# Performance work log

Measured on AMD Instinct MI355X. Metric: run time of the kernel, lower is better.

The kernel has to match this reference:

```python
import jax, jax.numpy as jnp
import numpy as np

GRID = (8192, 8192)   # 2D lattice, *dims
NDIM = 2              # links.shape[0]
P_LINK = 0.45         # subcritical bond probability -> finite clusters, bounded step count


def setup_inputs() -> dict:
    key = jax.random.key(0)
    k1, k2 = jax.random.split(key)
    # links[i] marks an open bond between site x and its +1 neighbour along axis i
    links = jax.random.uniform(k1, (NDIM,) + GRID) < P_LINK
    seed_idx = jax.random.randint(k2, (NDIM,), 0, GRID[0]).astype(jnp.int32)
    return {"links": links, "seed_idx": seed_idx}


def _flood_fill(links, seed_idx):
    """Faithful port of ClusterSelection.from_seed_idx: BFS-style roll+mask
    expansion iterated to fixed point via lax.while_loop."""
    ndim = links.shape[0]
    grid = links.shape[1:]
    selected0 = jnp.zeros(grid, dtype=bool).at[tuple(seed_idx)].set(True)

    def cond(carry):
        _, is_done, _ = carry
        return ~is_done

    def body(carry):
        sel0, _, steps = carry
        sel = sel0
        for i in range(ndim):  # unrolled over the (small, static) ndim
            # sites whose -1-neighbour or self is selected can use bond i
            links_to_try = sel0 | jnp.roll(sel0, -1, i)
            links_sel = links_to_try & links[i]
            # a taken bond marks both of its endpoints
            links_sel = links_sel | jnp.roll(links_sel, 1, i)
            sel = sel | links_sel
        is_done = (sel ^ sel0).sum() == 0
        return sel, is_done, steps + 1

    sel, _, steps = jax.lax.while_loop(
        cond, body, (selected0, jnp.array(False), jnp.array(0, jnp.int32))
    )
    return sel, steps


def reference(links, seed_idx):
    sel, _steps = _flood_fill(links, seed_idx)
    return sel
```

## Files before the change

kernel.cpp:

```cpp
#include <hip/hip_runtime.h>
#include <stdint.h>

#define GW 8192
#define GMASK 8191
#define PLANE 67108864ULL
#define TPD 128
#define TMASK 127
#define NTILES 16384
#define QCAP 16384
#define QMASK 16383
#define WPR 128

typedef unsigned long long u64;
typedef unsigned int u32;

__global__ void clear_bitmap_kernel(uint4* __restrict__ p, int n) {
    int i = blockIdx.x * blockDim.x + threadIdx.x;
    if (i < n) p[i] = make_uint4(0, 0, 0, 0);
}

__device__ __forceinline__ u32 nib4(u32 w) {
    return (((w & 0x01010101u) * 0x01020408u) >> 24) & 0xFu;
}
__device__ __forceinline__ u64 pack_row_b8(const unsigned char* p) {
    const uint4* q = (const uint4*)p;
    u64 w = 0;
#pragma unroll
    for (int i = 0; i < 4; i++) {
        uint4 v = q[i];
        u64 nb = (u64)(nib4(v.x) | (nib4(v.y) << 4) | (nib4(v.z) << 8) | (nib4(v.w) << 12));
        w |= nb << (16 * i);
    }
    return w;
}
__device__ __forceinline__ u64 pack_row_b32(const u32* p) {
    u64 w = 0;
#pragma unroll
    for (int k = 0; k < 16; k++) {
        uint4 v = ((const uint4*)p)[k];
        u64 nb = (u64)((v.x != 0) | ((v.y != 0) << 1) | ((v.z != 0) << 2) | ((v.w != 0) << 3));
        w |= nb << (4 * k);
    }
    return w;
}

__global__ void __launch_bounds__(1024)
bfs_tiles_kernel(const unsigned char* __restrict__ links8,
                 const int* __restrict__ seed_idx,
                 u64* __restrict__ bitmap) {
    volatile __shared__ unsigned short q[QCAP];
    __shared__ u32 tflags[NTILES / 32];
    __shared__ int s_qhead, s_qtail, s_active, s_mode, s_c1, s_c3;

    const int tid = threadIdx.x;
    const int ln  = tid & 63;

    for (int i = tid; i < QCAP; i += 1024) q[i] = 0xFFFF;
    for (int i = tid; i < NTILES / 32; i += 1024) tflags[i] = 0;
    if (tid == 0) { s_c1 = 0; s_c3 = 0; s_qhead = 0; s_qtail = 0; s_active = 0; }
    __syncthreads();

    int l1c = 0, l3c = 0;
    for (int i = tid; i < 16384; i += 1024) {
        if (links8[i]) { int m = i & 3; if (m == 1) l1c++; else if (m == 3) l3c++; }
    }
    atomicAdd(&s_c1, l1c);
    atomicAdd(&s_c3, l3c);
    __syncthreads();
    if (tid == 0) {
        s_mode = (s_c1 > 0) ? 0 : ((s_c3 > 0) ? 2 : 1);
        int sr = seed_idx[0] & GMASK, sc = seed_idx[1] & GMASK;
        atomicOr(&bitmap[(u64)sr * WPR + (sc >> 6)], 1ull << (sc & 63));
        int t = (sr >> 6) * TPD + (sc >> 6);
        tflags[t >> 5] = 1u << (t & 31);
        q[0] = (unsigned short)t;
        s_qtail = 1; s_active = 1;
    }
    __syncthreads();

    const int mode = s_mode;
    const unsigned char* p0b = links8;
    const unsigned char* p1b = links8 + PLANE;
    const u32* p0w = (const u32*)links8;
    const u32* p1w = (const u32*)(links8 + PLANE * 4);

    auto enq = [&](int t2) {
        u32 bit = 1u << (t2 & 31);
        u32 old = atomicOr(&tflags[t2 >> 5], bit);
        if (!(old & bit)) {
            atomicAdd(&s_active, 1);
            int pos = atomicAdd(&s_qtail, 1) & QMASK;
            q[pos] = (unsigned short)t2;
        }
    };

    long long guard = 0;
    while (true) {
        int t = -1;
        if (ln == 0) {
            while (true) {
                if (atomicAdd(&s_active, 0) == 0) break;
                int h  = atomicAdd(&s_qhead, 0);
                int tl = atomicAdd(&s_qtail, 0);
                if (h != tl && atomicCAS(&s_qhead, h, h + 1) == h) {
                    int pos = h & QMASK;
                    unsigned short v;
                    long long g2 = 0;
                    while ((v = q[pos]) == 0xFFFF) { if (++g2 > 400000000LL) break; }
                    q[pos] = 0xFFFF;
                    t = v;
                    break;
                }
                if (++guard > 400000000LL) break;
            }
        }
        t = __shfl(t, 0);
        if (t < 0) break;

        const int tR = t >> 7, tC = t & TMASK;
        if (ln == 0) atomicAnd(&tflags[t >> 5], ~(1u << (t & 31)));
        __threadfence_block();

        const int gr = tR * 64 + ln;
        u64* wp = &bitmap[(u64)gr * WPR + tC];
        u64 loaded = *(volatile u64*)wp;

        u64 l0, l1;
        if (mode == 0) {
            l0 = pack_row_b8(p0b + (u64)gr * GW + tC * 64);
            l1 = pack_row_b8(p1b + (u64)gr * GW + tC * 64);
        } else {
            l0 = pack_row_b32(p0w + (u64)gr * GW + tC * 64);
            l1 = pack_row_b32(p1w + (u64)gr * GW + tC * 64);
        }

        u64 P0 = l1 & 0x7FFFFFFFFFFFFFFFull;
        u64 P1 = P0 & (P0 >> 1);
        u64 P2 = P1 & (P1 >> 2);
        u64 P3 = P2 & (P2 >> 4);
        u64 P4 = P3 & (P3 >> 8);
        u64 P5 = P4 & (P4 >> 16);
        u64 D0 = (ln < 63) ? l0 : 0ull;
        u64 D1 = D0 & __shfl_down(D0, 1);
        u64 D2 = D1 & __shfl_down(D1, 2);
        u64 D3 = D2 & __shfl_down(D2, 4);
        u64 D4 = D3 & __shfl_down(D3, 8);
        u64 D5 = D4 & __shfl_down(D4, 16);

        u64 sel = loaded;
        while (true) {
            u64 old = sel;
            sel |= (sel & P0) << 1;  sel |= (sel >> 1)  & P0;
            sel |= (sel & P1) << 2;  sel |= (sel >> 2)  & P1;
            sel |= (sel & P2) << 4;  sel |= (sel >> 4)  & P2;
            sel |= (sel & P3) << 8;  sel |= (sel >> 8)  & P3;
            sel |= (sel & P4) << 16; sel |= (sel >> 16) & P4;
            sel |= (sel & P5) << 32; sel |= (sel >> 32) & P5;
            sel |= __shfl_up(sel & D0, 1);  sel |= __shfl_down(sel, 1)  & D0;
            sel |= __shfl_up(sel & D1, 2);  sel |= __shfl_down(sel, 2)  & D1;
            sel |= __shfl_up(sel & D2, 4);  sel |= __shfl_down(sel, 4)  & D2;
            sel |= __shfl_up(sel & D3, 8);  sel |= __shfl_down(sel, 8)  & D3;
            sel |= __shfl_up(sel & D4, 16); sel |= __shfl_down(sel, 16) & D4;
            sel |= __shfl_up(sel & D5, 32); sel |= __shfl_down(sel, 32) & D5;
            if (__ballot(sel != old) == 0ull) break;
        }

        u64 newbits = sel & ~loaded;
        if (newbits) atomicOr(wp, newbits);

        const int c0 = tC * 64;
        bool rnew = false, lnew = false;
        if ((sel >> 63) & (l1 >> 63) & 1ull) {
            u64 old = atomicOr(&bitmap[(u64)gr * WPR + ((tC + 1) & TMASK)], 1ull);
            rnew = !(old & 1ull);
        }
        {
            u64 lcol = (u64)((c0 - 1) & GMASK);
            bool lopen = (mode == 0) ? (p1b[(u64)gr * GW + lcol] != 0)
                                     : (p1w[(u64)gr * GW + lcol] != 0);
            if ((sel & 1ull) && lopen) {
                u64 old = atomicOr(&bitmap[(u64)gr * WPR + ((tC - 1) & TMASK)], 1ull << 63);
                lnew = !(old & (1ull << 63));
            }
        }
        u64 rmask = __ballot(rnew), lmask = __ballot(lnew);

        const int ga = (tR * 64 - 1) & GMASK;
        bool bopen = (mode == 0) ? (p0b[(u64)ga * GW + c0 + ln] != 0)
                                 : (p0w[(u64)ga * GW + c0 + ln] != 0);
        u64 top_sel = __shfl(sel, 0);
        u64 umask = __ballot(bopen && ((top_sel >> ln) & 1));
        u64 unew = 0;
        if (ln == 0 && umask) {
            u64 old = atomicOr(&bitmap[(u64)ga * WPR + tC], umask);
            unew = umask & ~old;
        }
        u64 dmask = sel & l0;
        const int gb = (tR * 64 + 64) & GMASK;
        u64 dnew = 0;
        if (ln == 63 && dmask) {
            u64 old = atomicOr(&bitmap[(u64)gb * WPR + tC], dmask);
            dnew = dmask & ~old;
        }

        if (ln == 0  && rmask) enq(tR * TPD + ((tC + 1) & TMASK));
        if (ln == 1  && lmask) enq(tR * TPD + ((tC - 1) & TMASK));
        if (ln == 0  && unew)  enq(((tR - 1) & TMASK) * TPD + tC);
        if (ln == 63 && dnew)  enq(((tR + 1) & TMASK) * TPD + tC);

        if (ln == 0) atomicSub(&s_active, 1);
    }
}

__global__ void writeout_kernel(const u64* __restrict__ bitmap, int4* __restrict__ out) {
    int g = blockIdx.x * blockDim.x + threadIdx.x;
    int site0 = g << 2;
    u64 w = bitmap[site0 >> 6];
    u32 b = (u32)(w >> (site0 & 63)) & 0xFu;
    out[g] = make_int4(b & 1, (b >> 1) & 1, (b >> 2) & 1, (b >> 3) & 1);
}

extern "C" void kernel_launch(void* const* d_in, const int* in_sizes, int n_in,
                              void* d_out, int out_size, void* d_ws, size_t ws_size,
                              hipStream_t stream) {
    const unsigned char* links = (const unsigned char*)d_in[0];
    const int* seed = (const int*)d_in[1];

    u64* bitmap = (u64*)((char*)d_ws + 4096);

    clear_bitmap_kernel<<<2048, 256, 0, stream>>>((uint4*)bitmap, 524288);
    bfs_tiles_kernel<<<1, 1024, 0, stream>>>(links, seed, bitmap);
    writeout_kernel<<<65536, 256, 0, stream>>>(bitmap, (int4*)d_out);
}
```

Before: 662.4 us.

## Fuse output zeroing with BFS and keep cluster tiles in shared memory

Replaces the separate bitmap clear and dense output writeout with one mega kernel. Block 0 runs the tile BFS on a shared-memory hash-indexed tile cache, while the other blocks zero the output and the global bitmap concurrently. The final writeout then touches only the visited tiles. If the cluster exceeds the slot capacity, a fallback path uses the global bitmap and a second BFS kernel. This adds spin-wait synchronisation between blocks and relies on the zeroing blocks finishing while block 0 is still resident.

```diff
diff --git a/kernel.cpp b/kernel.cpp
--- a/kernel.cpp
+++ b/kernel.cpp
@@ -7,17 +7,31 @@
 #define TPD 128
 #define TMASK 127
 #define NTILES 16384
+#define WPR 128
+
+#define NSLOT 224
+#define HCAP 1024
+#define HMASK 1023
+#define QC1 2048
+#define QM1 2047
+
 #define QCAP 16384
 #define QMASK 16383
-#define WPR 128
+
+#define WS_FILLDONE 0
+#define WS_OVER 8
+#define WS_GQN 16
+#define WS_NTILES 24
+#define WS_BITMAP 4096
+#define WS_LIST (WS_BITMAP + 8388608)
+#define WS_STAG (WS_LIST + 4096)
+#define WS_GQ (WS_STAG + NSLOT * 512)
+
+#define OUT_U4 16777216u
+#define BM_U4 524288u
 
 typedef unsigned long long u64;
 typedef unsigned int u32;
-
-__global__ void clear_bitmap_kernel(uint4* __restrict__ p, int n) {
-    int i = blockIdx.x * blockDim.x + threadIdx.x;
-    if (i < n) p[i] = make_uint4(0, 0, 0, 0);
-}
 
 __device__ __forceinline__ u32 nib4(u32 w) {
     return (((w & 0x01010101u) * 0x01020408u) >> 24) & 0xFu;
@@ -44,20 +58,51 @@
     return w;
 }
 
+__global__ void clear_ctrl_kernel(unsigned char* ws) {
+    if (threadIdx.x < 16) ((u32*)ws)[threadIdx.x] = 0;
+}
+
 __global__ void __launch_bounds__(1024)
-bfs_tiles_kernel(const unsigned char* __restrict__ links8,
-                 const int* __restrict__ seed_idx,
-                 u64* __restrict__ bitmap) {
-    volatile __shared__ unsigned short q[QCAP];
+mega_kernel(const unsigned char* __restrict__ links8,
+            const int* __restrict__ seed_idx,
+            unsigned char* __restrict__ ws,
+            uint4* __restrict__ outv) {
+    volatile __shared__ unsigned short q[QC1];
     __shared__ u32 tflags[NTILES / 32];
+    __shared__ u32 htab[HCAP];
+    __shared__ u64 selS[NSLOT][64];
+    __shared__ unsigned short slot_tile[NSLOT];
     __shared__ int s_qhead, s_qtail, s_active, s_mode, s_c1, s_c3;
+    __shared__ int s_nslots, s_over, s_gbready;
+
+    if (blockIdx.x != 0) {
+        u32 gtid = (blockIdx.x - 1) * 1024 + threadIdx.x;
+        u32 stride = (gridDim.x - 1) * 1024;
+        uint4 z = make_uint4(0, 0, 0, 0);
+        for (u32 i = gtid; i < OUT_U4; i += stride) outv[i] = z;
+        uint4* bm = (uint4*)(ws + WS_BITMAP);
+        for (u32 i = gtid; i < BM_U4; i += stride) bm[i] = z;
+        __syncthreads();
+        if (threadIdx.x == 0) {
+            __threadfence();
+            atomicAdd((u32*)(ws + WS_FILLDONE), 1u);
+        }
+        return;
+    }
 
     const int tid = threadIdx.x;
-    const int ln  = tid & 63;
-
-    for (int i = tid; i < QCAP; i += 1024) q[i] = 0xFFFF;
+    const int ln = tid & 63;
+    const int wv = tid >> 6;
+
+    for (int i = tid; i < QC1; i += 1024) q[i] = 0xFFFF;
     for (int i = tid; i < NTILES / 32; i += 1024) tflags[i] = 0;
-    if (tid == 0) { s_c1 = 0; s_c3 = 0; s_qhead = 0; s_qtail = 0; s_active = 0; }
+    for (int i = tid; i < HCAP; i += 1024) htab[i] = 0xFFFFFFFFu;
+    for (int i = tid; i < NSLOT; i += 1024) slot_tile[i] = 0xFFFF;
+    for (int i = tid; i < NSLOT * 64; i += 1024) ((u64*)selS)[i] = 0ull;
+    if (tid == 0) {
+        s_c1 = 0; s_c3 = 0; s_qhead = 0; s_qtail = 0; s_active = 0;
+        s_nslots = 0; s_over = 0; s_gbready = 0;
+    }
     __syncthreads();
 
     int l1c = 0, l3c = 0;
@@ -70,8 +115,12 @@
     if (tid == 0) {
         s_mode = (s_c1 > 0) ? 0 : ((s_c3 > 0) ? 2 : 1);
         int sr = seed_idx[0] & GMASK, sc = seed_idx[1] & GMASK;
-        atomicOr(&bitmap[(u64)sr * WPR + (sc >> 6)], 1ull << (sc & 63));
         int t = (sr >> 6) * TPD + (sc >> 6);
+        s_nslots = 1;
+        slot_tile[0] = (unsigned short)t;
+        u32 h = ((u32)t * 2654435761u) >> 22;
+        htab[h & HMASK] = (u32)t;
+        selS[0][sr & 63] = 1ull << (sc & 63);
         tflags[t >> 5] = 1u << (t & 31);
         q[0] = (unsigned short)t;
         s_qtail = 1; s_active = 1;
@@ -83,14 +132,58 @@
     const unsigned char* p1b = links8 + PLANE;
     const u32* p0w = (const u32*)links8;
     const u32* p1w = (const u32*)(links8 + PLANE * 4);
-
+    u64* bitmap = (u64*)(ws + WS_BITMAP);
+    const u32 nfill = gridDim.x - 1;
+
+    auto find_slot = [&](int t) -> int {
+        u32 h = ((u32)t * 2654435761u) >> 22;
+        for (int i = 0; i < HCAP; i++) {
+            u32 e = ((volatile u32*)htab)[(h + i) & HMASK];
+            if (e == 0xFFFFFFFFu) return -1;
+            if ((e & 0x3FFFu) == (u32)t) return (int)(e >> 14);
+        }
+        return -1;
+    };
+    auto find_or_alloc = [&](int t) -> int {
+        u32 h = ((u32)t * 2654435761u) >> 22;
+        for (int i = 0; i < HCAP; i++) {
+            int idx = (int)((h + i) & HMASK);
+            u32 e = ((volatile u32*)htab)[idx];
+            if (e == 0xFFFFFFFFu) {
+                int s = atomicAdd(&s_nslots, 1);
+                if (s >= NSLOT) { s_over = 1; return -1; }
+                u32 key = (u32)t | ((u32)s << 14);
+                u32 old = atomicCAS(&htab[idx], 0xFFFFFFFFu, key);
+                if (old == 0xFFFFFFFFu) { slot_tile[s] = (unsigned short)t; return s; }
+                if ((old & 0x3FFFu) == (u32)t) return (int)(old >> 14);
+            } else if ((e & 0x3FFFu) == (u32)t) {
+                return (int)(e >> 14);
+            }
+        }
+        s_over = 1; return -1;
+    };
     auto enq = [&](int t2) {
         u32 bit = 1u << (t2 & 31);
         u32 old = atomicOr(&tflags[t2 >> 5], bit);
         if (!(old & bit)) {
             atomicAdd(&s_active, 1);
-            int pos = atomicAdd(&s_qtail, 1) & QMASK;
+            int pos = atomicAdd(&s_qtail, 1) & QM1;
             q[pos] = (unsigned short)t2;
+        }
+    };
+    auto gq_enq = [&](int t2) {
+        u32 bit = 1u << (t2 & 31);
+        u32 old = atomicOr(&tflags[t2 >> 5], bit);
+        if (!(old & bit)) {
+            u32 p = atomicAdd((u32*)(ws + WS_GQN), 1u);
+            if (p < 16384u) ((u32*)(ws + WS_GQ))[p] = (u32)t2;
+        }
+    };
+    auto gb_wait = [&]() {
+        if (!s_gbready) {
+            while (atomicAdd((u32*)(ws + WS_FILLDONE), 0u) < nfill) {}
+            __threadfence();
+            s_gbready = 1;
         }
     };
 
@@ -100,10 +193,10 @@
         if (ln == 0) {
             while (true) {
                 if (atomicAdd(&s_active, 0) == 0) break;
-                int h  = atomicAdd(&s_qhead, 0);
+                int h = atomicAdd(&s_qhead, 0);
                 int tl = atomicAdd(&s_qtail, 0);
                 if (h != tl && atomicCAS(&s_qhead, h, h + 1) == h) {
-                    int pos = h & QMASK;
+                    int pos = h & QM1;
                     unsigned short v;
                     long long g2 = 0;
                     while ((v = q[pos]) == 0xFFFF) { if (++g2 > 400000000LL) break; }
@@ -118,12 +211,16 @@
         if (t < 0) break;
 
         const int tR = t >> 7, tC = t & TMASK;
+        int slot = -1;
+        if (ln == 0) slot = find_slot(t);
+        slot = __shfl(slot, 0);
+        if (slot < 0) { if (ln == 0) atomicSub(&s_active, 1); continue; }
+
         if (ln == 0) atomicAnd(&tflags[t >> 5], ~(1u << (t & 31)));
         __threadfence_block();
 
         const int gr = tR * 64 + ln;
-        u64* wp = &bitmap[(u64)gr * WPR + tC];
-        u64 loaded = *(volatile u64*)wp;
+        u64 loaded = *(volatile u64*)&selS[slot][ln];
 
         u64 l0, l1;
         if (mode == 0) {
@@ -166,6 +263,256 @@
         }
 
         u64 newbits = sel & ~loaded;
+        if (newbits) atomicOr(&selS[slot][ln], newbits);
+
+        const int c0 = tC * 64;
+        bool rcond = (((sel >> 63) & (l1 >> 63)) & 1ull) != 0;
+        u64 lcolb = (u64)((c0 - 1) & GMASK);
+        bool lopen = (mode == 0) ? (p1b[(u64)gr * GW + lcolb] != 0)
+                                 : (p1w[(u64)gr * GW + lcolb] != 0);
+        bool lcond = ((sel & 1ull) != 0) && lopen;
+        const int ga = (tR * 64 - 1) & GMASK;
+        bool bopen = (mode == 0) ? (p0b[(u64)ga * GW + c0 + ln] != 0)
+                                 : (p0w[(u64)ga * GW + c0 + ln] != 0);
+        u64 top_sel = __shfl(sel, 0);
+        u64 umask = __ballot(bopen && ((top_sel >> ln) & 1));
+        u64 dmask = sel & l0;
+        u64 dvote = __shfl(dmask, 63);
+        u64 rvote = __ballot(rcond);
+        u64 lvote = __ballot(lcond);
+
+        const int tRt = tR * TPD + ((tC + 1) & TMASK);
+        const int tLt = tR * TPD + ((tC - 1) & TMASK);
+        const int tUt = ((tR - 1) & TMASK) * TPD + tC;
+        const int tDt = ((tR + 1) & TMASK) * TPD + tC;
+
+        int sR = -2, sL = -2, sU = -2, sD = -2;
+        if (ln == 0) {
+            if (rvote) sR = find_or_alloc(tRt);
+            if (lvote) sL = find_or_alloc(tLt);
+            if (umask) sU = find_or_alloc(tUt);
+            if (dvote) sD = find_or_alloc(tDt);
+        }
+        sR = __shfl(sR, 0); sL = __shfl(sL, 0);
+        sU = __shfl(sU, 0); sD = __shfl(sD, 0);
+
+        bool rnew = false, lnew = false;
+        u64 unew = 0, dnew = 0;
+        if (rvote) {
+            if (sR >= 0) {
+                if (rcond) { u64 old = atomicOr(&selS[sR][ln], 1ull); rnew = !(old & 1ull); }
+            } else {
+                gb_wait();
+                if (rcond) {
+                    u64 old = atomicOr(&bitmap[(u64)gr * WPR + ((tC + 1) & TMASK)], 1ull);
+                    rnew = !(old & 1ull);
+                }
+            }
+        }
+        if (lvote) {
+            if (sL >= 0) {
+                if (lcond) { u64 old = atomicOr(&selS[sL][ln], 1ull << 63); lnew = !(old & (1ull << 63)); }
+            } else {
+                gb_wait();
+                if (lcond) {
+                    u64 old = atomicOr(&bitmap[(u64)gr * WPR + ((tC - 1) & TMASK)], 1ull << 63);
+                    lnew = !(old & (1ull << 63));
+                }
+            }
+        }
+        if (umask) {
+            if (sU >= 0) {
+                if (ln == 0) { u64 old = atomicOr(&selS[sU][63], umask); unew = umask & ~old; }
+            } else {
+                gb_wait();
+                if (ln == 0) { u64 old = atomicOr(&bitmap[(u64)ga * WPR + tC], umask); unew = umask & ~old; }
+            }
+        }
+        if (dvote) {
+            if (sD >= 0) {
+                if (ln == 63) { u64 old = atomicOr(&selS[sD][0], dmask); dnew = dmask & ~old; }
+            } else {
+                gb_wait();
+                if (ln == 63) {
+                    const int gb = (tR * 64 + 64) & GMASK;
+                    u64 old = atomicOr(&bitmap[(u64)gb * WPR + tC], dmask);
+                    dnew = dmask & ~old;
+                }
+            }
+        }
+        u64 rmask = __ballot(rnew), lmask = __ballot(lnew);
+
+        if (ln == 0  && rmask) { if (sR >= 0) enq(tRt); else gq_enq(tRt); }
+        if (ln == 1  && lmask) { if (sL >= 0) enq(tLt); else gq_enq(tLt); }
+        if (ln == 0  && unew)  { if (sU >= 0) enq(tUt); else gq_enq(tUt); }
+        if (ln == 63 && dnew)  { if (sD >= 0) enq(tDt); else gq_enq(tDt); }
+
+        if (ln == 0) atomicSub(&s_active, 1);
+    }
+
+    __syncthreads();
+    int ns = s_nslots; if (ns > NSLOT) ns = NSLOT;
+    int over = s_over;
+
+    if (over) {
+        if (tid == 0) {
+            while (atomicAdd((u32*)(ws + WS_FILLDONE), 0u) < nfill) {}
+            __threadfence();
+        }
+        __syncthreads();
+        for (int s = wv; s < ns; s += 16) {
+            int tt = slot_tile[s];
+            if (tt == 0xFFFF) continue;
+            u64 w = selS[s][ln];
+            if (w) atomicOr(&bitmap[(u64)((tt >> 7) * 64 + ln) * WPR + (tt & TMASK)], w);
+        }
+    } else {
+        u64* stag = (u64*)(ws + WS_STAG);
+        for (int s = wv; s < ns; s += 16) stag[s * 64 + ln] = selS[s][ln];
+    }
+    for (int i = tid; i < ns; i += 1024)
+        ((u32*)(ws + WS_LIST))[i] = (u32)slot_tile[i];
+    if (tid == 0) {
+        *(u32*)(ws + WS_NTILES) = (u32)ns;
+        *(u32*)(ws + WS_OVER) = (u32)over;
+    }
+}
+
+__global__ void __launch_bounds__(1024)
+fb_bfs_kernel(const unsigned char* __restrict__ links8,
+              unsigned char* __restrict__ ws) {
+    __shared__ int s_go;
+    volatile __shared__ unsigned short q[QCAP];
+    __shared__ u32 tflags[NTILES / 32];
+    __shared__ int s_qhead, s_qtail, s_active, s_mode, s_c1, s_c3;
+
+    if (threadIdx.x == 0) s_go = (int)*(volatile u32*)(ws + WS_OVER);
+    __syncthreads();
+    if (!s_go) return;
+
+    const int tid = threadIdx.x;
+    const int ln = tid & 63;
+    u64* bitmap = (u64*)(ws + WS_BITMAP);
+
+    for (int i = tid; i < QCAP; i += 1024) q[i] = 0xFFFF;
+    for (int i = tid; i < NTILES / 32; i += 1024) tflags[i] = 0;
+    if (tid == 0) { s_c1 = 0; s_c3 = 0; s_qhead = 0; s_qtail = 0; s_active = 0; }
+    __syncthreads();
+
+    int l1c = 0, l3c = 0;
+    for (int i = tid; i < 16384; i += 1024) {
+        if (links8[i]) { int m = i & 3; if (m == 1) l1c++; else if (m == 3) l3c++; }
+    }
+    atomicAdd(&s_c1, l1c);
+    atomicAdd(&s_c3, l3c);
+    __syncthreads();
+    if (tid == 0) s_mode = (s_c1 > 0) ? 0 : ((s_c3 > 0) ? 2 : 1);
+    __syncthreads();
+
+    {
+        u32 ntl = *(u32*)(ws + WS_NTILES);
+        u32 gqn = *(u32*)(ws + WS_GQN); if (gqn > 16384u) gqn = 16384u;
+        const u32* listp = (const u32*)(ws + WS_LIST);
+        const u32* gqp = (const u32*)(ws + WS_GQ);
+        for (u32 i = tid; i < ntl + gqn; i += 1024) {
+            u32 tt = (i < ntl) ? listp[i] : gqp[i - ntl];
+            if (tt == 0xFFFFu) continue;
+            int pos = atomicAdd(&s_qtail, 1) & QMASK;
+            q[pos] = (unsigned short)tt;
+            atomicAdd(&s_active, 1);
+            atomicOr(&tflags[tt >> 5], 1u << (tt & 31));
+        }
+    }
+    __syncthreads();
+
+    const int mode = s_mode;
+    const unsigned char* p0b = links8;
+    const unsigned char* p1b = links8 + PLANE;
+    const u32* p0w = (const u32*)links8;
+    const u32* p1w = (const u32*)(links8 + PLANE * 4);
+
+    auto enq = [&](int t2) {
+        u32 bit = 1u << (t2 & 31);
+        u32 old = atomicOr(&tflags[t2 >> 5], bit);
+        if (!(old & bit)) {
+            atomicAdd(&s_active, 1);
+            int pos = atomicAdd(&s_qtail, 1) & QMASK;
+            q[pos] = (unsigned short)t2;
+        }
+    };
+
+    long long guard = 0;
+    while (true) {
+        int t = -1;
+        if (ln == 0) {
+            while (true) {
+                if (atomicAdd(&s_active, 0) == 0) break;
+                int h = atomicAdd(&s_qhead, 0);
+                int tl = atomicAdd(&s_qtail, 0);
+                if (h != tl && atomicCAS(&s_qhead, h, h + 1) == h) {
+                    int pos = h & QMASK;
+                    unsigned short v;
+                    long long g2 = 0;
+                    while ((v = q[pos]) == 0xFFFF) { if (++g2 > 400000000LL) break; }
+                    q[pos] = 0xFFFF;
+                    t = v;
+                    break;
+                }
+                if (++guard > 400000000LL) break;
+            }
+        }
+        t = __shfl(t, 0);
+        if (t < 0) break;
+
+        const int tR = t >> 7, tC = t & TMASK;
+        if (ln == 0) atomicAnd(&tflags[t >> 5], ~(1u << (t & 31)));
+        __threadfence_block();
+
+        const int gr = tR * 64 + ln;
+        u64* wp = &bitmap[(u64)gr * WPR + tC];
+        u64 loaded = *(volatile u64*)wp;
+
+        u64 l0, l1;
+        if (mode == 0) {
+            l0 = pack_row_b8(p0b + (u64)gr * GW + tC * 64);
+            l1 = pack_row_b8(p1b + (u64)gr * GW + tC * 64);
+        } else {
+            l0 = pack_row_b32(p0w + (u64)gr * GW + tC * 64);
+            l1 = pack_row_b32(p1w + (u64)gr * GW + tC * 64);
+        }
+
+        u64 P0 = l1 & 0x7FFFFFFFFFFFFFFFull;
+        u64 P1 = P0 & (P0 >> 1);
+        u64 P2 = P1 & (P1 >> 2);
+        u64 P3 = P2 & (P2 >> 4);
+        u64 P4 = P3 & (P3 >> 8);
+        u64 P5 = P4 & (P4 >> 16);
+        u64 D0 = (ln < 63) ? l0 : 0ull;
+        u64 D1 = D0 & __shfl_down(D0, 1);
+        u64 D2 = D1 & __shfl_down(D1, 2);
+        u64 D3 = D2 & __shfl_down(D2, 4);
+        u64 D4 = D3 & __shfl_down(D3, 8);
+        u64 D5 = D4 & __shfl_down(D4, 16);
+
+        u64 sel = loaded;
+        while (true) {
+            u64 old = sel;
+            sel |= (sel & P0) << 1;  sel |= (sel >> 1)  & P0;
+            sel |= (sel & P1) << 2;  sel |= (sel >> 2)  & P1;
+            sel |= (sel & P2) << 4;  sel |= (sel >> 4)  & P2;
+            sel |= (sel & P3) << 8;  sel |= (sel >> 8)  & P3;
+            sel |= (sel & P4) << 16; sel |= (sel >> 16) & P4;
+            sel |= (sel & P5) << 32; sel |= (sel >> 32) & P5;
+            sel |= __shfl_up(sel & D0, 1);  sel |= __shfl_down(sel, 1)  & D0;
+            sel |= __shfl_up(sel & D1, 2);  sel |= __shfl_down(sel, 2)  & D1;
+            sel |= __shfl_up(sel & D2, 4);  sel |= __shfl_down(sel, 4)  & D2;
+            sel |= __shfl_up(sel & D3, 8);  sel |= __shfl_down(sel, 8)  & D3;
+            sel |= __shfl_up(sel & D4, 16); sel |= __shfl_down(sel, 16) & D4;
+            sel |= __shfl_up(sel & D5, 32); sel |= __shfl_down(sel, 32) & D5;
+            if (__ballot(sel != old) == 0ull) break;
+        }
+
+        u64 newbits = sel & ~loaded;
         if (newbits) atomicOr(wp, newbits);
 
         const int c0 = tC * 64;
@@ -212,12 +559,45 @@
     }
 }
 
-__global__ void writeout_kernel(const u64* __restrict__ bitmap, int4* __restrict__ out) {
-    int g = blockIdx.x * blockDim.x + threadIdx.x;
-    int site0 = g << 2;
-    u64 w = bitmap[site0 >> 6];
-    u32 b = (u32)(w >> (site0 & 63)) & 0xFu;
-    out[g] = make_int4(b & 1, (b >> 1) & 1, (b >> 2) & 1, (b >> 3) & 1);
+__global__ void writeout_kernel(const unsigned char* __restrict__ ws,
+                                int* __restrict__ out) {
+    __shared__ u32 s_over, s_n;
+    if (threadIdx.x == 0) {
+        s_over = *(volatile u32*)(ws + WS_OVER);
+        s_n = *(volatile u32*)(ws + WS_NTILES);
+    }
+    __syncthreads();
+
+    if (s_over) {
+        const u64* bitmap = (const u64*)(ws + WS_BITMAP);
+        u32 nth = gridDim.x * blockDim.x;
+        u32 gt = blockIdx.x * blockDim.x + threadIdx.x;
+        for (u32 i = gt; i < 1048576u; i += nth) {
+            u64 w = bitmap[i];
+            if (!w) continue;
+            u64 base = (u64)i << 6;
+            while (w) {
+                int b = __ffsll((unsigned long long)w) - 1;
+                out[base + b] = 1;
+                w &= w - 1;
+            }
+        }
+        return;
+    }
+
+    if (blockIdx.x >= s_n) return;
+    u32 tt = ((const u32*)(ws + WS_LIST))[blockIdx.x];
+    if (tt == 0xFFFFu) return;
+    const u64* stag = (const u64*)(ws + WS_STAG);
+    const int trr = (int)(tt >> 7), tcc = (int)(tt & TMASK);
+    int4* ob = (int4*)out;
+    for (int i = threadIdx.x; i < 1024; i += 256) {
+        int row = i >> 4, c4 = i & 15;
+        u64 w = stag[(u64)blockIdx.x * 64 + row];
+        u32 nb = (u32)(w >> (c4 * 4)) & 0xFu;
+        ob[(u64)(trr * 64 + row) * 2048 + tcc * 16 + c4] =
+            make_int4(nb & 1, (nb >> 1) & 1, (nb >> 2) & 1, (nb >> 3) & 1);
+    }
 }
 
 extern "C" void kernel_launch(void* const* d_in, const int* in_sizes, int n_in,
@@ -225,10 +605,10 @@
                               hipStream_t stream) {
     const unsigned char* links = (const unsigned char*)d_in[0];
     const int* seed = (const int*)d_in[1];
-
-    u64* bitmap = (u64*)((char*)d_ws + 4096);
-
-    clear_bitmap_kernel<<<2048, 256, 0, stream>>>((uint4*)bitmap, 524288);
-    bfs_tiles_kernel<<<1, 1024, 0, stream>>>(links, seed, bitmap);
-    writeout_kernel<<<65536, 256, 0, stream>>>(bitmap, (int4*)d_out);
-}
+    unsigned char* ws = (unsigned char*)d_ws;
+
+    clear_ctrl_kernel<<<1, 64, 0, stream>>>(ws);
+    mega_kernel<<<2049, 1024, 0, stream>>>(links, seed, ws, (uint4*)d_out);
+    fb_bfs_kernel<<<1, 1024, 0, stream>>>(links, ws);
+    writeout_kernel<<<NSLOT, 256, 0, stream>>>(ws, (int*)d_out);
+}
```

Result: slower. 721.2 us (+8.9%).

## Widen BFS tiles to 64x256 with four-word fill and halve block size

Applied to the files above, without the earlier changes.

Each wavefront now processes a 64-row by 256-column tile held as four 64-bit words per lane, instead of a 64x64 tile. Horizontal fill runs per word, with cross-word carries between neighbouring words, followed by vertical shuffle fill. The aim is fewer queue operations and tile dequeues, at the cost of more registers per lane. The persistent single block drops from 1024 to 512 threads, which reduces parallel tile workers and risks more idle work on tiles that touch only part of the cluster.

```diff
diff --git a/kernel.cpp b/kernel.cpp
--- a/kernel.cpp
+++ b/kernel.cpp
@@ -4,12 +4,15 @@
 #define GW 8192
 #define GMASK 8191
 #define PLANE 67108864ULL
-#define TPD 128
-#define TMASK 127
-#define NTILES 16384
+#define WPR 128
+
+#define TPR 128
+#define TRMASK 127
+#define TPC 32
+#define TCMASK 31
+#define NTILES 4096
 #define QCAP 16384
 #define QMASK 16383
-#define WPR 128
 
 typedef unsigned long long u64;
 typedef unsigned int u32;
@@ -44,7 +47,38 @@
     return w;
 }
 
-__global__ void __launch_bounds__(1024)
+#define HFILL(S, Pa, Pb, Pc, Pd, Pe, Pf) \
+    S |= (S & Pa) << 1;  S |= (S >> 1)  & Pa; \
+    S |= (S & Pb) << 2;  S |= (S >> 2)  & Pb; \
+    S |= (S & Pc) << 4;  S |= (S >> 4)  & Pc; \
+    S |= (S & Pd) << 8;  S |= (S >> 8)  & Pd; \
+    S |= (S & Pe) << 16; S |= (S >> 16) & Pe; \
+    S |= (S & Pf) << 32; S |= (S >> 32) & Pf;
+
+#define VFILL(S, Da, Db, Dc, Dd, De, Df) \
+    S |= __shfl_up(S & Da, 1);  S |= __shfl_down(S, 1)  & Da; \
+    S |= __shfl_up(S & Db, 2);  S |= __shfl_down(S, 2)  & Db; \
+    S |= __shfl_up(S & Dc, 4);  S |= __shfl_down(S, 4)  & Dc; \
+    S |= __shfl_up(S & Dd, 8);  S |= __shfl_down(S, 8)  & Dd; \
+    S |= __shfl_up(S & De, 16); S |= __shfl_down(S, 16) & De; \
+    S |= __shfl_up(S & Df, 32); S |= __shfl_down(S, 32) & Df;
+
+#define MKP(l, P0, P1, P2, P3, P4, P5) \
+    u64 P0 = (l) & 0x7FFFFFFFFFFFFFFFull; \
+    u64 P1 = P0 & (P0 >> 1);  u64 P2 = P1 & (P1 >> 2); \
+    u64 P3 = P2 & (P2 >> 4);  u64 P4 = P3 & (P3 >> 8); \
+    u64 P5 = P4 & (P4 >> 16);
+
+#define MKD(l, D0, D1, D2, D3, D4, D5) \
+    u64 D0 = (ln < 63) ? (l) : 0ull; \
+    u64 D1 = D0 & __shfl_down(D0, 1);  u64 D2 = D1 & __shfl_down(D1, 2); \
+    u64 D3 = D2 & __shfl_down(D2, 4);  u64 D4 = D3 & __shfl_down(D3, 8); \
+    u64 D5 = D4 & __shfl_down(D4, 16);
+
+#define XW(Sa, Sb, bond) \
+    Sb |= (Sa >> 63) & (bond); Sa |= ((Sb & 1ull) & (bond)) << 63;
+
+__global__ void __launch_bounds__(512)
 bfs_tiles_kernel(const unsigned char* __restrict__ links8,
                  const int* __restrict__ seed_idx,
                  u64* __restrict__ bitmap) {
@@ -55,13 +89,13 @@
     const int tid = threadIdx.x;
     const int ln  = tid & 63;
 
-    for (int i = tid; i < QCAP; i += 1024) q[i] = 0xFFFF;
-    for (int i = tid; i < NTILES / 32; i += 1024) tflags[i] = 0;
+    for (int i = tid; i < QCAP; i += 512) q[i] = 0xFFFF;
+    for (int i = tid; i < NTILES / 32; i += 512) tflags[i] = 0;
     if (tid == 0) { s_c1 = 0; s_c3 = 0; s_qhead = 0; s_qtail = 0; s_active = 0; }
     __syncthreads();
 
     int l1c = 0, l3c = 0;
-    for (int i = tid; i < 16384; i += 1024) {
+    for (int i = tid; i < 16384; i += 512) {
         if (links8[i]) { int m = i & 3; if (m == 1) l1c++; else if (m == 3) l3c++; }
     }
     atomicAdd(&s_c1, l1c);
@@ -71,7 +105,7 @@
         s_mode = (s_c1 > 0) ? 0 : ((s_c3 > 0) ? 2 : 1);
         int sr = seed_idx[0] & GMASK, sc = seed_idx[1] & GMASK;
         atomicOr(&bitmap[(u64)sr * WPR + (sc >> 6)], 1ull << (sc & 63));
-        int t = (sr >> 6) * TPD + (sc >> 6);
+        int t = (sr >> 6) * TPC + (sc >> 8);
         tflags[t >> 5] = 1u << (t & 31);
         q[0] = (unsigned short)t;
         s_qtail = 1; s_active = 1;
@@ -117,96 +151,140 @@
         t = __shfl(t, 0);
         if (t < 0) break;
 
-        const int tR = t >> 7, tC = t & TMASK;
+        const int tR = t >> 5, tCc = t & TCMASK;
         if (ln == 0) atomicAnd(&tflags[t >> 5], ~(1u << (t & 31)));
         __threadfence_block();
 
         const int gr = tR * 64 + ln;
-        u64* wp = &bitmap[(u64)gr * WPR + tC];
-        u64 loaded = *(volatile u64*)wp;
-
-        u64 l0, l1;
+        const int c0 = tCc * 256;
+        const int w0 = tCc * 4;
+        u64* wp = &bitmap[(u64)gr * WPR + w0];
+        u64 ld0v = ((volatile u64*)wp)[0];
+        u64 ld1v = ((volatile u64*)wp)[1];
+        u64 ld2v = ((volatile u64*)wp)[2];
+        u64 ld3v = ((volatile u64*)wp)[3];
+
+        u64 l0_0, l0_1, l0_2, l0_3;
+        u64 l1_0, l1_1, l1_2, l1_3;
         if (mode == 0) {
-            l0 = pack_row_b8(p0b + (u64)gr * GW + tC * 64);
-            l1 = pack_row_b8(p1b + (u64)gr * GW + tC * 64);
+            const unsigned char* r0 = p0b + (u64)gr * GW + c0;
+            const unsigned char* r1 = p1b + (u64)gr * GW + c0;
+            l0_0 = pack_row_b8(r0);       l0_1 = pack_row_b8(r0 + 64);
+            l0_2 = pack_row_b8(r0 + 128); l0_3 = pack_row_b8(r0 + 192);
+            l1_0 = pack_row_b8(r1);       l1_1 = pack_row_b8(r1 + 64);
+            l1_2 = pack_row_b8(r1 + 128); l1_3 = pack_row_b8(r1 + 192);
         } else {
-            l0 = pack_row_b32(p0w + (u64)gr * GW + tC * 64);
-            l1 = pack_row_b32(p1w + (u64)gr * GW + tC * 64);
-        }
-
-        u64 P0 = l1 & 0x7FFFFFFFFFFFFFFFull;
-        u64 P1 = P0 & (P0 >> 1);
-        u64 P2 = P1 & (P1 >> 2);
-        u64 P3 = P2 & (P2 >> 4);
-        u64 P4 = P3 & (P3 >> 8);
-        u64 P5 = P4 & (P4 >> 16);
-        u64 D0 = (ln < 63) ? l0 : 0ull;
-        u64 D1 = D0 & __shfl_down(D0, 1);
-        u64 D2 = D1 & __shfl_down(D1, 2);
-        u64 D3 = D2 & __shfl_down(D2, 4);
-        u64 D4 = D3 & __shfl_down(D3, 8);
-        u64 D5 = D4 & __shfl_down(D4, 16);
-
-        u64 sel = loaded;
+            const u32* r0 = p0w + (u64)gr * GW + c0;
+            const u32* r1 = p1w + (u64)gr * GW + c0;
+            l0_0 = pack_row_b32(r0);       l0_1 = pack_row_b32(r0 + 64);
+            l0_2 = pack_row_b32(r0 + 128); l0_3 = pack_row_b32(r0 + 192);
+            l1_0 = pack_row_b32(r1);       l1_1 = pack_row_b32(r1 + 64);
+            l1_2 = pack_row_b32(r1 + 128); l1_3 = pack_row_b32(r1 + 192);
+        }
+
+        const u64 cw01 = (l1_0 >> 63) & 1ull;
+        const u64 cw12 = (l1_1 >> 63) & 1ull;
+        const u64 cw23 = (l1_2 >> 63) & 1ull;
+        const bool rbond = ((l1_3 >> 63) & 1ull) != 0;
+
+        MKP(l1_0, P0_0, P1_0, P2_0, P3_0, P4_0, P5_0);
+        MKP(l1_1, P0_1, P1_1, P2_1, P3_1, P4_1, P5_1);
+        MKP(l1_2, P0_2, P1_2, P2_2, P3_2, P4_2, P5_2);
+        MKP(l1_3, P0_3, P1_3, P2_3, P3_3, P4_3, P5_3);
+        MKD(l0_0, D0_0, D1_0, D2_0, D3_0, D4_0, D5_0);
+        MKD(l0_1, D0_1, D1_1, D2_1, D3_1, D4_1, D5_1);
+        MKD(l0_2, D0_2, D1_2, D2_2, D3_2, D4_2, D5_2);
+        MKD(l0_3, D0_3, D1_3, D2_3, D3_3, D4_3, D5_3);
+
+        u64 sel0 = ld0v, sel1 = ld1v, sel2 = ld2v, sel3 = ld3v;
         while (true) {
-            u64 old = sel;
-            sel |= (sel & P0) << 1;  sel |= (sel >> 1)  & P0;
-            sel |= (sel & P1) << 2;  sel |= (sel >> 2)  & P1;
-            sel |= (sel & P2) << 4;  sel |= (sel >> 4)  & P2;
-            sel |= (sel & P3) << 8;  sel |= (sel >> 8)  & P3;
-            sel |= (sel & P4) << 16; sel |= (sel >> 16) & P4;
-            sel |= (sel & P5) << 32; sel |= (sel >> 32) & P5;
-            sel |= __shfl_up(sel & D0, 1);  sel |= __shfl_down(sel, 1)  & D0;
-            sel |= __shfl_up(sel & D1, 2);  sel |= __shfl_down(sel, 2)  & D1;
-            sel |= __shfl_up(sel & D2, 4);  sel |= __shfl_down(sel, 4)  & D2;
-            sel |= __shfl_up(sel & D3, 8);  sel |= __shfl_down(sel, 8)  & D3;
-            sel |= __shfl_up(sel & D4, 16); sel |= __shfl_down(sel, 16) & D4;
-            sel |= __shfl_up(sel & D5, 32); sel |= __shfl_down(sel, 32) & D5;
-            if (__ballot(sel != old) == 0ull) break;
-        }
-
-        u64 newbits = sel & ~loaded;
-        if (newbits) atomicOr(wp, newbits);
-
-        const int c0 = tC * 64;
-        bool rnew = false, lnew = false;
-        if ((sel >> 63) & (l1 >> 63) & 1ull) {
-            u64 old = atomicOr(&bitmap[(u64)gr * WPR + ((tC + 1) & TMASK)], 1ull);
+            u64 o0 = sel0, o1 = sel1, o2 = sel2, o3 = sel3;
+            HFILL(sel0, P0_0, P1_0, P2_0, P3_0, P4_0, P5_0);
+            HFILL(sel1, P0_1, P1_1, P2_1, P3_1, P4_1, P5_1);
+            HFILL(sel2, P0_2, P1_2, P2_2, P3_2, P4_2, P5_2);
+            HFILL(sel3, P0_3, P1_3, P2_3, P3_3, P4_3, P5_3);
+            XW(sel0, sel1, cw01);
+            XW(sel1, sel2, cw12);
+            XW(sel2, sel3, cw23);
+            XW(sel1, sel2, cw12);
+            XW(sel0, sel1, cw01);
+            VFILL(sel0, D0_0, D1_0, D2_0, D3_0, D4_0, D5_0);
+            VFILL(sel1, D0_1, D1_1, D2_1, D3_1, D4_1, D5_1);
+            VFILL(sel2, D0_2, D1_2, D2_2, D3_2, D4_2, D5_2);
+            VFILL(sel3, D0_3, D1_3, D2_3, D3_3, D4_3, D5_3);
+            u64 ch = (sel0 ^ o0) | (sel1 ^ o1) | (sel2 ^ o2) | (sel3 ^ o3);
+            if (__ballot(ch != 0ull) == 0ull) break;
+        }
+
+        u64 nb0 = sel0 & ~ld0v; if (nb0) atomicOr(wp + 0, nb0);
+        u64 nb1 = sel1 & ~ld1v; if (nb1) atomicOr(wp + 1, nb1);
+        u64 nb2 = sel2 & ~ld2v; if (nb2) atomicOr(wp + 2, nb2);
+        u64 nb3 = sel3 & ~ld3v; if (nb3) atomicOr(wp + 3, nb3);
+
+        bool rnew = false;
+        if (((sel3 >> 63) & 1ull) && rbond) {
+            u64 old = atomicOr(&bitmap[(u64)gr * WPR + ((tCc + 1) & TCMASK) * 4], 1ull);
             rnew = !(old & 1ull);
         }
-        {
+        bool lnew = false;
+        if (sel0 & 1ull) {
             u64 lcol = (u64)((c0 - 1) & GMASK);
             bool lopen = (mode == 0) ? (p1b[(u64)gr * GW + lcol] != 0)
                                      : (p1w[(u64)gr * GW + lcol] != 0);
-            if ((sel & 1ull) && lopen) {
-                u64 old = atomicOr(&bitmap[(u64)gr * WPR + ((tC - 1) & TMASK)], 1ull << 63);
+            if (lopen) {
+                u64 old = atomicOr(&bitmap[(u64)gr * WPR + ((tCc - 1) & TCMASK) * 4 + 3],
+                                   1ull << 63);
                 lnew = !(old & (1ull << 63));
             }
         }
         u64 rmask = __ballot(rnew), lmask = __ballot(lnew);
 
         const int ga = (tR * 64 - 1) & GMASK;
-        bool bopen = (mode == 0) ? (p0b[(u64)ga * GW + c0 + ln] != 0)
-                                 : (p0w[(u64)ga * GW + c0 + ln] != 0);
-        u64 top_sel = __shfl(sel, 0);
-        u64 umask = __ballot(bopen && ((top_sel >> ln) & 1));
+        u64 um0 = 0, um1 = 0, um2 = 0, um3 = 0;
+        {
+            u64 ts;
+            ts = __shfl(sel0, 0);
+            if (ts) um0 = __ballot(((ts >> ln) & 1) &&
+                ((mode == 0) ? (p0b[(u64)ga * GW + c0 + ln] != 0)
+                             : (p0w[(u64)ga * GW + c0 + ln] != 0)));
+            ts = __shfl(sel1, 0);
+            if (ts) um1 = __ballot(((ts >> ln) & 1) &&
+                ((mode == 0) ? (p0b[(u64)ga * GW + c0 + 64 + ln] != 0)
+                             : (p0w[(u64)ga * GW + c0 + 64 + ln] != 0)));
+            ts = __shfl(sel2, 0);
+            if (ts) um2 = __ballot(((ts >> ln) & 1) &&
+                ((mode == 0) ? (p0b[(u64)ga * GW + c0 + 128 + ln] != 0)
+                             : (p0w[(u64)ga * GW + c0 + 128 + ln] != 0)));
+            ts = __shfl(sel3, 0);
+            if (ts) um3 = __ballot(((ts >> ln) & 1) &&
+                ((mode == 0) ? (p0b[(u64)ga * GW + c0 + 192 + ln] != 0)
+                             : (p0w[(u64)ga * GW + c0 + 192 + ln] != 0)));
+        }
+        u64 myum = (ln == 0) ? um0 : (ln == 1) ? um1 : (ln == 2) ? um2 : (ln == 3) ? um3 : 0;
         u64 unew = 0;
-        if (ln == 0 && umask) {
-            u64 old = atomicOr(&bitmap[(u64)ga * WPR + tC], umask);
-            unew = umask & ~old;
-        }
-        u64 dmask = sel & l0;
+        if (ln < 4 && myum) {
+            u64 old = atomicOr(&bitmap[(u64)ga * WPR + w0 + ln], myum);
+            unew = myum & ~old;
+        }
+        u64 uany = __ballot(unew != 0);
+
         const int gb = (tR * 64 + 64) & GMASK;
+        u64 dm0 = __shfl(sel0 & l0_0, 63);
+        u64 dm1 = __shfl(sel1 & l0_1, 63);
+        u64 dm2 = __shfl(sel2 & l0_2, 63);
+        u64 dm3 = __shfl(sel3 & l0_3, 63);
+        u64 mydm = (ln == 4) ? dm0 : (ln == 5) ? dm1 : (ln == 6) ? dm2 : (ln == 7) ? dm3 : 0;
         u64 dnew = 0;
-        if (ln == 63 && dmask) {
-            u64 old = atomicOr(&bitmap[(u64)gb * WPR + tC], dmask);
-            dnew = dmask & ~old;
-        }
-
-        if (ln == 0  && rmask) enq(tR * TPD + ((tC + 1) & TMASK));
-        if (ln == 1  && lmask) enq(tR * TPD + ((tC - 1) & TMASK));
-        if (ln == 0  && unew)  enq(((tR - 1) & TMASK) * TPD + tC);
-        if (ln == 63 && dnew)  enq(((tR + 1) & TMASK) * TPD + tC);
+        if (ln >= 4 && ln < 8 && mydm) {
+            u64 old = atomicOr(&bitmap[(u64)gb * WPR + w0 + (ln - 4)], mydm);
+            dnew = mydm & ~old;
+        }
+        u64 dany = __ballot(dnew != 0);
+
+        if (ln == 0 && rmask) enq(tR * TPC + ((tCc + 1) & TCMASK));
+        if (ln == 1 && lmask) enq(tR * TPC + ((tCc - 1) & TCMASK));
+        if (ln == 2 && uany)  enq(((tR - 1) & TRMASK) * TPC + tCc);
+        if (ln == 3 && dany)  enq(((tR + 1) & TRMASK) * TPC + tCc);
 
         if (ln == 0) atomicSub(&s_active, 1);
     }
@@ -229,6 +307,6 @@
     u64* bitmap = (u64*)((char*)d_ws + 4096);
 
     clear_bitmap_kernel<<<2048, 256, 0, stream>>>((uint4*)bitmap, 524288);
-    bfs_tiles_kernel<<<1, 1024, 0, stream>>>(links, seed, bitmap);
+    bfs_tiles_kernel<<<1, 512, 0, stream>>>(links, seed, bitmap);
     writeout_kernel<<<65536, 256, 0, stream>>>(bitmap, (int4*)d_out);
 }
```

Result: slower. 679.8 us (+2.6%).

## Overlap output zeroing with BFS and write out only visited tiles

Applied to the files above, without the earlier changes.

Merges output zero-fill into the BFS launch: extra blocks zero the 256MB int32 output while block 0 runs the single-block tile BFS. The BFS records every tile ever enqueued, and a sparse writeout then converts only those tiles' bitmap bits to int32. This replaces a full 256MB read-convert-write pass. It also skips halo link loads when the edge bits are empty. The risk is that the zeroing blocks compete with the BFS block for memory bandwidth.

```diff
diff --git a/kernel.cpp b/kernel.cpp
--- a/kernel.cpp
+++ b/kernel.cpp
@@ -11,6 +11,11 @@
 #define QMASK 16383
 #define WPR 128
 
+#define WS_BITMAP 4096
+#define WS_TFEVER (WS_BITMAP + 8388608)
+
+#define OUT_U4 16777216u
+
 typedef unsigned long long u64;
 typedef unsigned int u32;
 
@@ -45,18 +50,29 @@
 }
 
 __global__ void __launch_bounds__(1024)
-bfs_tiles_kernel(const unsigned char* __restrict__ links8,
-                 const int* __restrict__ seed_idx,
-                 u64* __restrict__ bitmap) {
+mega_kernel(const unsigned char* __restrict__ links8,
+            const int* __restrict__ seed_idx,
+            unsigned char* __restrict__ ws,
+            uint4* __restrict__ outv) {
     volatile __shared__ unsigned short q[QCAP];
     __shared__ u32 tflags[NTILES / 32];
+    __shared__ u32 tfever[NTILES / 32];
     __shared__ int s_qhead, s_qtail, s_active, s_mode, s_c1, s_c3;
 
+    if (blockIdx.x != 0) {
+        u32 gtid = (blockIdx.x - 1) * 1024 + threadIdx.x;
+        u32 stride = (gridDim.x - 1) * 1024;
+        uint4 z = make_uint4(0, 0, 0, 0);
+        for (u32 i = gtid; i < OUT_U4; i += stride) outv[i] = z;
+        return;
+    }
+
+    u64* bitmap = (u64*)(ws + WS_BITMAP);
     const int tid = threadIdx.x;
     const int ln  = tid & 63;
 
     for (int i = tid; i < QCAP; i += 1024) q[i] = 0xFFFF;
-    for (int i = tid; i < NTILES / 32; i += 1024) tflags[i] = 0;
+    for (int i = tid; i < NTILES / 32; i += 1024) { tflags[i] = 0; tfever[i] = 0; }
     if (tid == 0) { s_c1 = 0; s_c3 = 0; s_qhead = 0; s_qtail = 0; s_active = 0; }
     __syncthreads();
 
@@ -73,6 +89,7 @@
         atomicOr(&bitmap[(u64)sr * WPR + (sc >> 6)], 1ull << (sc & 63));
         int t = (sr >> 6) * TPD + (sc >> 6);
         tflags[t >> 5] = 1u << (t & 31);
+        tfever[t >> 5] = 1u << (t & 31);
         q[0] = (unsigned short)t;
         s_qtail = 1; s_active = 1;
     }
@@ -86,6 +103,7 @@
 
     auto enq = [&](int t2) {
         u32 bit = 1u << (t2 & 31);
+        atomicOr(&tfever[t2 >> 5], bit);
         u32 old = atomicOr(&tflags[t2 >> 5], bit);
         if (!(old & bit)) {
             atomicAdd(&s_active, 1);
@@ -174,11 +192,11 @@
             u64 old = atomicOr(&bitmap[(u64)gr * WPR + ((tC + 1) & TMASK)], 1ull);
             rnew = !(old & 1ull);
         }
-        {
+        if (sel & 1ull) {
             u64 lcol = (u64)((c0 - 1) & GMASK);
             bool lopen = (mode == 0) ? (p1b[(u64)gr * GW + lcol] != 0)
                                      : (p1w[(u64)gr * GW + lcol] != 0);
-            if ((sel & 1ull) && lopen) {
+            if (lopen) {
                 u64 old = atomicOr(&bitmap[(u64)gr * WPR + ((tC - 1) & TMASK)], 1ull << 63);
                 lnew = !(old & (1ull << 63));
             }
@@ -186,10 +204,14 @@
         u64 rmask = __ballot(rnew), lmask = __ballot(lnew);
 
         const int ga = (tR * 64 - 1) & GMASK;
-        bool bopen = (mode == 0) ? (p0b[(u64)ga * GW + c0 + ln] != 0)
-                                 : (p0w[(u64)ga * GW + c0 + ln] != 0);
         u64 top_sel = __shfl(sel, 0);
-        u64 umask = __ballot(bopen && ((top_sel >> ln) & 1));
+        u64 umask = 0;
+        if (top_sel) {
+            bool bopen = ((top_sel >> ln) & 1) &&
+                ((mode == 0) ? (p0b[(u64)ga * GW + c0 + ln] != 0)
+                             : (p0w[(u64)ga * GW + c0 + ln] != 0));
+            umask = __ballot(bopen);
+        }
         u64 unew = 0;
         if (ln == 0 && umask) {
             u64 old = atomicOr(&bitmap[(u64)ga * WPR + tC], umask);
@@ -210,14 +232,27 @@
 
         if (ln == 0) atomicSub(&s_active, 1);
     }
-}
-
-__global__ void writeout_kernel(const u64* __restrict__ bitmap, int4* __restrict__ out) {
-    int g = blockIdx.x * blockDim.x + threadIdx.x;
-    int site0 = g << 2;
-    u64 w = bitmap[site0 >> 6];
-    u32 b = (u32)(w >> (site0 & 63)) & 0xFu;
-    out[g] = make_int4(b & 1, (b >> 1) & 1, (b >> 2) & 1, (b >> 3) & 1);
+
+    __syncthreads();
+    for (int i = tid; i < NTILES / 32; i += 1024)
+        ((u32*)(ws + WS_TFEVER))[i] = tfever[i];
+}
+
+__global__ void __launch_bounds__(256)
+writeout_sparse(const unsigned char* __restrict__ ws, int4* __restrict__ ob) {
+    const u64* bitmap = (const u64*)(ws + WS_BITMAP);
+    const u32* tf = (const u32*)(ws + WS_TFEVER);
+    for (int t = blockIdx.x; t < NTILES; t += gridDim.x) {
+        if (!((tf[t >> 5] >> (t & 31)) & 1u)) continue;
+        int tR = t >> 7, tC = t & TMASK;
+        for (int i = threadIdx.x; i < 1024; i += 256) {
+            int row = i >> 4, c4 = i & 15;
+            u64 w = bitmap[(u64)(tR * 64 + row) * WPR + tC];
+            u32 nb = (u32)(w >> (c4 * 4)) & 0xFu;
+            ob[(u64)(tR * 64 + row) * 2048 + tC * 16 + c4] =
+                make_int4(nb & 1, (nb >> 1) & 1, (nb >> 2) & 1, (nb >> 3) & 1);
+        }
+    }
 }
 
 extern "C" void kernel_launch(void* const* d_in, const int* in_sizes, int n_in,
@@ -225,10 +260,11 @@
                               hipStream_t stream) {
     const unsigned char* links = (const unsigned char*)d_in[0];
     const int* seed = (const int*)d_in[1];
-
-    u64* bitmap = (u64*)((char*)d_ws + 4096);
+    unsigned char* ws = (unsigned char*)d_ws;
+
+    u64* bitmap = (u64*)(ws + WS_BITMAP);
 
     clear_bitmap_kernel<<<2048, 256, 0, stream>>>((uint4*)bitmap, 524288);
-    bfs_tiles_kernel<<<1, 1024, 0, stream>>>(links, seed, bitmap);
-    writeout_kernel<<<65536, 256, 0, stream>>>(bitmap, (int4*)d_out);
-}
+    mega_kernel<<<513, 1024, 0, stream>>>(links, seed, ws, (uint4*)d_out);
+    writeout_sparse<<<1024, 256, 0, stream>>>(ws, (int4*)d_out);
+}
```

Result: no change. 654.2 us, median of 2 (-1.2%).
